# Kernel tuning notes

Measured on AMD Instinct MI355X. Metric: run time of the kernel, lower is better.

The kernel has to match this reference:

```python
import jax, jax.numpy as jnp
import numpy as np

N = 50000
E = 800000
NFEAT = 128
NHID = 64
NCLASS = 40


def setup_inputs() -> dict:
    key = jax.random.key(0)
    ks = jax.random.split(key, 12)
    return {
        "x": jax.random.normal(ks[0], (N, NFEAT), dtype=jnp.float32),
        "M": jax.random.uniform(ks[1], (N, 1), dtype=jnp.float32),
        "AM": jax.random.uniform(ks[2], (N, 1), dtype=jnp.float32),
        "adj_vals": jax.random.uniform(ks[3], (E,), dtype=jnp.float32),
        "adjZ_vals": jax.random.uniform(ks[4], (E,), dtype=jnp.float32),
        "W0": jax.random.normal(ks[5], (NFEAT, NFEAT), dtype=jnp.float32) * (1.414 / np.sqrt(NFEAT)),
        "b0": jnp.zeros((NFEAT,), dtype=jnp.float32),
        "W1": jax.random.normal(ks[6], (NFEAT, NHID), dtype=jnp.float32) * (1.414 / np.sqrt(NFEAT)),
        "b1": jnp.zeros((NHID,), dtype=jnp.float32),
        "W2": jax.random.normal(ks[7], (NHID, NCLASS), dtype=jnp.float32) * (1.0 / np.sqrt(NHID)),
        "b2": jnp.zeros((NCLASS,), dtype=jnp.float32),
        "row": jax.random.randint(ks[8], (E,), 0, N, dtype=jnp.int32),
        "col": jax.random.randint(ks[9], (E,), 0, N, dtype=jnp.int32),
    }


def _spmm(vals, row, col, X, n):
    # sparse (COO) @ dense: out[r] = sum_e vals[e] * X[col[e]] for row[e]==r
    return jax.ops.segment_sum(vals[:, None] * X[col], row, num_segments=n)


def reference(x, M, AM, adj_vals, adjZ_vals, W0, b0, W1, b1, W2, b2, row, col):
    n = x.shape[0]
    # gc0: PaGConv(nfeat->nfeat) on adjZ, then ReLU (dropout is identity in eval)
    h = _spmm(adjZ_vals, row, col, M * x, n) * AM
    h = jax.nn.relu(h @ W0 + b0)
    # gc1: PaGConv(nfeat->nhid) on adjZ, then ReLU
    h = _spmm(adjZ_vals, row, col, M * h, n) * AM
    h = jax.nn.relu(h @ W1 + b1)
    # gc2: plain GConv(nhid->nclass) on adj
    h = _spmm(adj_vals, row, col, h, n)
    h = h @ W2 + b2
    return jax.nn.log_softmax(h, axis=1)
```

## Files before the change

kernel.cpp:

```cpp
#include <hip/hip_runtime.h>
#include <hip/hip_bf16.h>
#include <math.h>


typedef __attribute__((ext_vector_type(8))) short bf16x8;
typedef __attribute__((ext_vector_type(4))) float f32x4;

#define HIST_EPB_LOG 15
#define HIST_EPB 32768
#define NBINS 50176
#define NBMAX 26
#define SCAN_BLOCKS 196

__device__ __forceinline__ float rl_f(float v, int j) {
    return __builtin_bit_cast(float,
        __builtin_amdgcn_readlane(__builtin_bit_cast(int, v), j));
}
__device__ __forceinline__ int rl_i(int v, int j) {
    return __builtin_amdgcn_readlane(v, j);
}
__device__ __forceinline__ unsigned short f2bf(float f) {
    unsigned u = __builtin_bit_cast(unsigned, f);
    u += 0x7fffu + ((u >> 16) & 1u);
    return (unsigned short)(u >> 16);
}
__device__ __forceinline__ unsigned pack2bf(float lo, float hi) {
    return (unsigned)f2bf(lo) | ((unsigned)f2bf(hi) << 16);
}
__device__ __forceinline__ float bf_lo(unsigned u) {
    return __builtin_bit_cast(float, u << 16);
}
__device__ __forceinline__ float bf_hi(unsigned u) {
    return __builtin_bit_cast(float, u & 0xffff0000u);
}
__device__ __forceinline__ float clampf(float v) {
    return fminf(fmaxf(v, -1e30f), 1e30f);
}


__global__ void prep_wt(const float* __restrict__ W0, const float* __restrict__ W1,
                        const float* __restrict__ W2,
                        unsigned short* __restrict__ wt0, unsigned short* __restrict__ wt1,
                        unsigned short* __restrict__ wt2) {
    int idx = blockIdx.x * 256 + threadIdx.x;
    if (idx < 128 * 128) {
        int nn = idx >> 7, k = idx & 127;
        wt0[idx] = f2bf(W0[k * 128 + nn]);
    }
    idx -= 128 * 128;
    if (idx >= 0 && idx < 64 * 128) {
        int nn = idx >> 7, k = idx & 127;
        wt1[idx] = f2bf(W1[k * 64 + nn]);
    }
    idx -= 64 * 128;
    if (idx >= 0 && idx < 48 * 64) {
        int nn = idx >> 6, k = idx & 63;
        wt2[idx] = (nn < 40) ? f2bf(W2[k * 40 + nn]) : (unsigned short)0;
    }
}


template <int K, int COLS, int NTPAD, bool ABF16, bool MSCALE>
__device__ __forceinline__ void gemm_mfma_body(const void* __restrict__ Asrc,
                                               const float* __restrict__ Mv,
                                               const unsigned short* __restrict__ Wt,
                                               unsigned short* __restrict__ outp,
                                               int n, int bid, int tid) {
    constexpr int KS = K / 32;
    const int lane = tid & 63;
    const int wid = tid >> 6;
    const int m15 = lane & 15;
    const int q = lane >> 4;
    const int rA = bid * 64 + wid * 16 + m15;

    bf16x8 a[KS];
    if constexpr (ABF16) {
        const unsigned short* A = (const unsigned short*)Asrc;
#pragma unroll
        for (int ks = 0; ks < KS; ++ks) {
            uint4 z = make_uint4(0u, 0u, 0u, 0u);
            if (rA < n) z = *(const uint4*)(A + (size_t)rA * K + ks * 32 + q * 8);
            a[ks] = __builtin_bit_cast(bf16x8, z);
        }
    } else {
        const float* A = (const float*)Asrc;
        float m = 1.0f;
        if constexpr (MSCALE) { if (rA < n) m = Mv[rA]; }
#pragma unroll
        for (int ks = 0; ks < KS; ++ks) {
            float4 lo = make_float4(0.f, 0.f, 0.f, 0.f);
            float4 hi = make_float4(0.f, 0.f, 0.f, 0.f);
            if (rA < n) {
                lo = *(const float4*)(A + (size_t)rA * K + ks * 32 + q * 8);
                hi = *(const float4*)(A + (size_t)rA * K + ks * 32 + q * 8 + 4);
            }
            union { bf16x8 v; unsigned short u[8]; } pk;
            pk.u[0] = f2bf(lo.x * m); pk.u[1] = f2bf(lo.y * m);
            pk.u[2] = f2bf(lo.z * m); pk.u[3] = f2bf(lo.w * m);
            pk.u[4] = f2bf(hi.x * m); pk.u[5] = f2bf(hi.y * m);
            pk.u[6] = f2bf(hi.z * m); pk.u[7] = f2bf(hi.w * m);
            a[ks] = pk.v;
        }
    }

#pragma unroll
    for (int nt = 0; nt < NTPAD / 16; ++nt) {
        f32x4 acc = {0.f, 0.f, 0.f, 0.f};
        const int bn = nt * 16 + m15;
#pragma unroll
        for (int ks = 0; ks < KS; ++ks) {
            const uint4 z = *(const uint4*)(Wt + (size_t)bn * K + ks * 32 + q * 8);
            const bf16x8 b = __builtin_bit_cast(bf16x8, z);
            acc = __builtin_amdgcn_mfma_f32_16x16x32_bf16(a[ks], b, acc, 0, 0, 0);
        }
        const int gc = nt * 16 + m15;
#pragma unroll
        for (int rr = 0; rr < 4; ++rr) {
            const int gr = bid * 64 + wid * 16 + q * 4 + rr;
            bool ok = gr < n;
            if constexpr (NTPAD != COLS) ok = ok && (gc < COLS);
            if (ok) outp[(size_t)gr * COLS + gc] = f2bf(clampf(acc[rr]));
        }
    }
}

template <int K, int COLS, int NTPAD, bool ABF16, bool MSCALE>
__launch_bounds__(256)
__global__ void gemm_mfma(const void* __restrict__ A, const float* __restrict__ Mv,
                          const unsigned short* __restrict__ Wt,
                          unsigned short* __restrict__ out, int n) {
    gemm_mfma_body<K, COLS, NTPAD, ABF16, MSCALE>(A, Mv, Wt, out, n, blockIdx.x,
                                                  threadIdx.x);
}


__launch_bounds__(1024)
__global__ void hist_gemm0(const int* __restrict__ row,
                           unsigned short* __restrict__ cntmat,
                           unsigned short* __restrict__ lrank, int E, int NB,
                           const float* __restrict__ x, const float* __restrict__ Mv,
                           const unsigned short* __restrict__ Wt0,
                           unsigned short* __restrict__ t_buf, int n) {
    __shared__ __align__(16) unsigned hcnt[NBINS / 2];
    const int blk = blockIdx.x;
    const int t = threadIdx.x;
    if (blk < NB) {
        uint4* h4 = (uint4*)hcnt;
        const uint4 z4 = make_uint4(0u, 0u, 0u, 0u);
        for (int i = t; i < NBINS / 8; i += 1024) h4[i] = z4;
        __syncthreads();
        const int s = blk << HIST_EPB_LOG;
        const int e = min(E, s + HIST_EPB);
        for (int i = s + t; i < e; i += 1024) {
            const int r = row[i];
            const unsigned sh = (unsigned)(r & 1) << 4;
            const unsigned old = atomicAdd(&hcnt[r >> 1], 1u << sh);
            lrank[i] = (unsigned short)((old >> sh) & 0xffffu);
        }
        __syncthreads();
        uint4* dst = (uint4*)(cntmat + (size_t)blk * NBINS);
        for (int i = t; i < NBINS / 8; i += 1024) dst[i] = h4[i];
    } else {
        const int sub = t >> 8;
        gemm_mfma_body<128, 128, 128, false, true>(x, Mv, Wt0, t_buf, n,
                                                   (blk - NB) * 4 + sub, t & 255);
    }
}


__launch_bounds__(256)
__global__ void scan_one(const unsigned short* __restrict__ cm,
                         unsigned* __restrict__ cmabs, int* __restrict__ rp,
                         unsigned long long* __restrict__ gpub,
                         int n, int NB, int E) {
    __shared__ int sd[256];
    const int g = blockIdx.x;
    const int t = threadIdx.x;
    const int bin = g * 256 + t;

    unsigned tot = 0;
    for (int b = 0; b < NB; ++b) tot += cm[(size_t)b * NBINS + bin];

    sd[t] = (int)tot;
    __syncthreads();
    for (int off = 1; off < 256; off <<= 1) {
        int xv = (t >= off) ? sd[t - off] : 0;
        __syncthreads();
        sd[t] += xv;
        __syncthreads();
    }
    const int excl = sd[t] - (int)tot;
    const int gtot = sd[255];
    __syncthreads();

    if (t == 0)
        atomicExch(&gpub[g], (1ULL << 32) | (unsigned long long)(unsigned)gtot);

    int my = 0;
    for (int p = t; p < g; p += 256) {
        unsigned long long v;
        do { v = atomicAdd(&gpub[p], 0ULL); } while ((v >> 32) == 0ULL);
        my += (int)(unsigned)v;
    }
    sd[t] = my;
    __syncthreads();
    for (int off = 128; off > 0; off >>= 1) {
        if (t < off) sd[t] += sd[t + off];
        __syncthreads();
    }
    const int base = sd[0];

    const int rpf = base + excl;
    if (bin < n) rp[bin] = rpf;
    if (g == SCAN_BLOCKS - 1 && t == 255) rp[n] = E;

    int run = rpf;
    for (int b = 0; b < NB; ++b) {
        cmabs[(size_t)b * NBINS + bin] = (unsigned)run;
        run += (int)cm[(size_t)b * NBINS + bin];
    }
}


__global__ void scatter_kernel(const int* __restrict__ row, const int* __restrict__ col,
                               const float* __restrict__ vA, const float* __restrict__ vZ,
                               const unsigned* __restrict__ cmabs,
                               const unsigned short* __restrict__ lrank,
                               uint4* __restrict__ packed16, int E) {
    int e = blockIdx.x * blockDim.x + threadIdx.x;
    if (e >= E) return;
    const int r = row[e];
    const int pos = (int)(cmabs[(size_t)(e >> HIST_EPB_LOG) * NBINS + r]
                          + (unsigned)lrank[e]);
    uint4 pk;
    pk.x = (unsigned)col[e];
    pk.y = __builtin_bit_cast(unsigned, vZ[e]);
    pk.z = __builtin_bit_cast(unsigned, vA[e]);
    pk.w = 0u;
    packed16[pos] = pk;
}


__launch_bounds__(256)
__global__ void spmm128_kernel(const uint4* __restrict__ packed16,
                               const int* __restrict__ rp, const unsigned short* __restrict__ X,
                               const float* __restrict__ AM, const float* __restrict__ Mv,
                               const float* __restrict__ bias,
                               unsigned short* __restrict__ out, int n) {
    const int lane = threadIdx.x & 63;
    const int r = (int)((blockIdx.x * (unsigned)blockDim.x + threadIdx.x) >> 6);
    if (r >= n) return;
    const int s = __builtin_amdgcn_readfirstlane(rp[r]);
    const int e = __builtin_amdgcn_readfirstlane(rp[r + 1]);

    float acc0 = 0.0f, acc1 = 0.0f;
    for (int base = s; base < e; base += 64) {
        const int nn = min(64, e - base);
        int ci = 0; float vf = 0.0f;
        if (lane < nn) {
            const uint4 pk = packed16[base + lane];
            ci = (int)pk.x;
            vf = __builtin_bit_cast(float, pk.y);
        }
        int j = 0;
        for (; j + 16 <= nn; j += 16) {
            unsigned u[16];
#pragma unroll
            for (int q = 0; q < 16; ++q) {
                const int cq = rl_i(ci, j + q);
                u[q] = *(const unsigned*)(X + (size_t)cq * 128 + lane * 2);
            }
#pragma unroll
            for (int q = 0; q < 16; ++q) {
                const float vq = rl_f(vf, j + q);
                acc0 += vq * bf_lo(u[q]);
                acc1 += vq * bf_hi(u[q]);
            }
        }
        for (; j + 8 <= nn; j += 8) {
            unsigned u[8];
#pragma unroll
            for (int q = 0; q < 8; ++q) {
                const int cq = rl_i(ci, j + q);
                u[q] = *(const unsigned*)(X + (size_t)cq * 128 + lane * 2);
            }
#pragma unroll
            for (int q = 0; q < 8; ++q) {
                const float vq = rl_f(vf, j + q);
                acc0 += vq * bf_lo(u[q]);
                acc1 += vq * bf_hi(u[q]);
            }
        }
        for (; j < nn; ++j) {
            const int cq = rl_i(ci, j);
            const float vq = rl_f(vf, j);
            const unsigned u = *(const unsigned*)(X + (size_t)cq * 128 + lane * 2);
            acc0 += vq * bf_lo(u);
            acc1 += vq * bf_hi(u);
        }
    }

    const float am = AM[r];
    const float mr = Mv[r];
    const float o0 = fminf(fmaxf((acc0 * am + bias[2 * lane]) * mr, 0.0f), 1e30f);
    const float o1 = fminf(fmaxf((acc1 * am + bias[2 * lane + 1]) * mr, 0.0f), 1e30f);
    ((unsigned*)out)[(size_t)r * 64 + lane] = pack2bf(o0, o1);
}


__launch_bounds__(256)
__global__ void spmm64_kernel(const uint4* __restrict__ packed16,
                              const int* __restrict__ rp, const unsigned short* __restrict__ X,
                              const float* __restrict__ AM, const float* __restrict__ bias,
                              unsigned short* __restrict__ out, int n) {
    const int lane = threadIdx.x & 63;
    const int g = lane >> 4;
    const int ls = lane & 15;
    const int r = (int)((blockIdx.x * (unsigned)blockDim.x + threadIdx.x) >> 6);
    if (r >= n) return;
    const int s = __builtin_amdgcn_readfirstlane(rp[r]);
    const int e = __builtin_amdgcn_readfirstlane(rp[r + 1]);

    float a0 = 0.0f, a1 = 0.0f, a2 = 0.0f, a3 = 0.0f;
    for (int base = s; base < e; base += 64) {
        const int nn = min(64, e - base);
        int ci = 0; float vf = 0.0f;
        if (lane < nn) {
            const uint4 pk = packed16[base + lane];
            ci = (int)pk.x;
            vf = __builtin_bit_cast(float, pk.y);
        }
        for (int j = 0; j < nn; j += 16) {
#pragma unroll
            for (int q = 0; q < 4; ++q) {
                const int jj = j + 4 * q + g;
                const bool ok = jj < nn;
                const int idx = jj & 63;
                const int c = __shfl(ci, idx);
                const float v = __shfl(vf, idx);
                if (ok) {
                    const uint2 u = *(const uint2*)(X + (size_t)c * 64 + ls * 4);
                    a0 += v * bf_lo(u.x);
                    a1 += v * bf_hi(u.x);
                    a2 += v * bf_lo(u.y);
                    a3 += v * bf_hi(u.y);
                }
            }
        }
    }
    a0 += __shfl_xor(a0, 16); a0 += __shfl_xor(a0, 32);
    a1 += __shfl_xor(a1, 16); a1 += __shfl_xor(a1, 32);
    a2 += __shfl_xor(a2, 16); a2 += __shfl_xor(a2, 32);
    a3 += __shfl_xor(a3, 16); a3 += __shfl_xor(a3, 32);

    if (lane < 16) {
        const float am = AM[r];
        const float o0 = fminf(fmaxf(a0 * am + bias[4 * ls + 0], 0.0f), 1e30f);
        const float o1 = fminf(fmaxf(a1 * am + bias[4 * ls + 1], 0.0f), 1e30f);
        const float o2 = fminf(fmaxf(a2 * am + bias[4 * ls + 2], 0.0f), 1e30f);
        const float o3 = fminf(fmaxf(a3 * am + bias[4 * ls + 3], 0.0f), 1e30f);
        uint2 w;
        w.x = pack2bf(o0, o1);
        w.y = pack2bf(o2, o3);
        *(uint2*)((unsigned*)out + (size_t)r * 32 + ls * 2) = w;
    }
}


__launch_bounds__(256)
__global__ void spmm40_kernel(const uint4* __restrict__ packed16,
                              const int* __restrict__ rp, const unsigned short* __restrict__ X,
                              const float* __restrict__ bias,
                              float* __restrict__ out, int n) {
    const int lane = threadIdx.x & 63;
    const int g = lane / 20;
    const int ls = lane - 20 * g;
    const bool active = g < 3;
    const int r = (int)((blockIdx.x * (unsigned)blockDim.x + threadIdx.x) >> 6);
    if (r >= n) return;
    const int s = __builtin_amdgcn_readfirstlane(rp[r]);
    const int e = __builtin_amdgcn_readfirstlane(rp[r + 1]);

    float acc0 = 0.0f, acc1 = 0.0f;
    for (int base = s; base < e; base += 64) {
        const int nn = min(64, e - base);
        int ci = 0; float vf = 0.0f;
        if (lane < nn) {
            const uint4 pk = packed16[base + lane];
            ci = (int)pk.x;
            vf = __builtin_bit_cast(float, pk.z);
        }
        for (int j = 0; j < nn; j += 24) {
#pragma unroll
            for (int q = 0; q < 8; ++q) {
                const int jj = j + 3 * q + g;
                const bool ok = active && jj < nn;
                const int idx = jj & 63;
                const int c = __shfl(ci, idx);
                const float v = __shfl(vf, idx);
                if (ok) {
                    const unsigned u = *(const unsigned*)(X + (size_t)c * 40 + ls * 2);
                    acc0 += v * bf_lo(u);
                    acc1 += v * bf_hi(u);
                }
            }
        }
    }
    {
        const float a1 = __shfl(acc0, (lane + 20) & 63);
        const float a2 = __shfl(acc0, (lane + 40) & 63);
        const float b1 = __shfl(acc1, (lane + 20) & 63);
        const float b2 = __shfl(acc1, (lane + 40) & 63);
        acc0 += a1 + a2;
        acc1 += b1 + b2;
    }

    const bool own = lane < 20;
    const float vv0 = own ? fminf(fmaxf(acc0 + bias[2 * ls], -1e30f), 1e30f) : -INFINITY;
    const float vv1 = own ? fminf(fmaxf(acc1 + bias[2 * ls + 1], -1e30f), 1e30f) : -INFINITY;
    float mx = fmaxf(vv0, vv1);
#pragma unroll
    for (int off = 32; off > 0; off >>= 1) mx = fmaxf(mx, __shfl_xor(mx, off));
    float sum = own ? (expf(vv0 - mx) + expf(vv1 - mx)) : 0.0f;
#pragma unroll
    for (int off = 32; off > 0; off >>= 1) sum += __shfl_xor(sum, off);
    if (own) {
        const float lse = mx + logf(sum);
        *(float2*)(out + (size_t)r * 40 + ls * 2) = make_float2(vv0 - lse, vv1 - lse);
    }
}


extern "C" void kernel_launch(void* const* d_in, const int* in_sizes, int n_in,
                              void* d_out, int out_size, void* d_ws, size_t ws_size,
                              hipStream_t stream) {
    const float* x    = (const float*)d_in[0];
    const float* M    = (const float*)d_in[1];
    const float* AM   = (const float*)d_in[2];
    const float* adjv = (const float*)d_in[3];
    const float* adjZ = (const float*)d_in[4];
    const float* W0   = (const float*)d_in[5];
    const float* b0   = (const float*)d_in[6];
    const float* W1   = (const float*)d_in[7];
    const float* b1   = (const float*)d_in[8];
    const float* W2   = (const float*)d_in[9];
    const float* b2   = (const float*)d_in[10];
    const int* row    = (const int*)d_in[11];
    const int* col    = (const int*)d_in[12];
    float* out = (float*)d_out;

    const int n = in_sizes[1];
    const int E = in_sizes[3];

    unsigned short* t_buf = (unsigned short*)d_ws;
    unsigned short* wt0 = t_buf + (size_t)n * 128;
    unsigned short* wt1 = wt0 + 128 * 128;
    unsigned short* wt2 = wt1 + 64 * 128;
    unsigned short* h_buf = wt2 + 48 * 64;
    unsigned short* lrank  = h_buf;
    unsigned short* cntmat = lrank + (size_t)E;
    unsigned* cmabs = (unsigned*)(cntmat + (size_t)NBMAX * NBINS);
    int* rp = (int*)(h_buf + (size_t)n * 128);
    unsigned long long* gpub = (unsigned long long*)
        (((uintptr_t)(rp + n + 2) + 7) & ~(uintptr_t)7);
    uint4* packed16 = (uint4*)
        (((uintptr_t)(gpub + 256) + 15) & ~(uintptr_t)15);

    const int NB = (E + HIST_EPB - 1) >> HIST_EPB_LOG;
    const int gemmBlocks = (n + 63) / 64;
    const int gemmB4 = (gemmBlocks + 3) / 4;

    hipMemsetAsync(gpub, 0, 256 * sizeof(unsigned long long), stream);
    prep_wt<<<(128 * 128 + 64 * 128 + 48 * 64 + 255) / 256, 256, 0, stream>>>(
        W0, W1, W2, wt0, wt1, wt2);

    hist_gemm0<<<NB + gemmB4, 1024, 0, stream>>>(row, cntmat, lrank, E, NB,
                                                 x, M, wt0, t_buf, n);

    scan_one<<<SCAN_BLOCKS, 256, 0, stream>>>(cntmat, cmabs, rp, gpub, n, NB, E);

    scatter_kernel<<<(E + 255) / 256, 256, 0, stream>>>(row, col, adjv, adjZ,
                                                        cmabs, lrank, packed16, E);

    const int spmmBlocks = (n + 3) / 4;

    spmm128_kernel<<<spmmBlocks, 256, 0, stream>>>(packed16, rp, t_buf, AM, M, b0, h_buf, n);
    gemm_mfma<128, 64, 64, true, false><<<gemmBlocks, 256, 0, stream>>>(h_buf, nullptr, wt1,
                                                                        t_buf, n);
    spmm64_kernel<<<spmmBlocks, 256, 0, stream>>>(packed16, rp, t_buf, AM, b1, h_buf, n);
    gemm_mfma<64, 40, 48, true, false><<<gemmBlocks, 256, 0, stream>>>(h_buf, nullptr, wt2,
                                                                       t_buf, n);
    spmm40_kernel<<<spmmBlocks, 256, 0, stream>>>(packed16, rp, t_buf, b2, out, n);
}
```

Baseline: 271.7 us.

## Fuse weight prep, scan+scatter, and spmm64 with gemm2 to cut launches

Folds the bf16 weight-transpose into block 0 of the histogram/gemm0 kernel, with the gemm0 blocks spin-waiting on a flag before reading the weights. Merges the prefix scan and the edge scatter into one persistent-style kernel that waits on a global counter. Fuses the final 64->40 projection into the spmm64 kernel using readlane broadcasts, so one gemm launch and one intermediate round-trip are dropped. Cross-block spin-waits rely on all blocks being co-resident or scheduled in order, which adds deadlock risk and some idle spinning.

```diff
diff --git a/kernel.cpp b/kernel.cpp
--- a/kernel.cpp
+++ b/kernel.cpp
@@ -11,6 +11,7 @@
 #define NBINS 50176
 #define NBMAX 26
 #define SCAN_BLOCKS 196
+#define SS_GRID 1568
 
 __device__ __forceinline__ float rl_f(float v, int j) {
     return __builtin_bit_cast(float,
@@ -38,34 +39,11 @@
 }
 
 
-__global__ void prep_wt(const float* __restrict__ W0, const float* __restrict__ W1,
-                        const float* __restrict__ W2,
-                        unsigned short* __restrict__ wt0, unsigned short* __restrict__ wt1,
-                        unsigned short* __restrict__ wt2) {
-    int idx = blockIdx.x * 256 + threadIdx.x;
-    if (idx < 128 * 128) {
-        int nn = idx >> 7, k = idx & 127;
-        wt0[idx] = f2bf(W0[k * 128 + nn]);
-    }
-    idx -= 128 * 128;
-    if (idx >= 0 && idx < 64 * 128) {
-        int nn = idx >> 7, k = idx & 127;
-        wt1[idx] = f2bf(W1[k * 64 + nn]);
-    }
-    idx -= 64 * 128;
-    if (idx >= 0 && idx < 48 * 64) {
-        int nn = idx >> 6, k = idx & 63;
-        wt2[idx] = (nn < 40) ? f2bf(W2[k * 40 + nn]) : (unsigned short)0;
-    }
-}
-
-
-template <int K, int COLS, int NTPAD, bool ABF16, bool MSCALE>
-__device__ __forceinline__ void gemm_mfma_body(const void* __restrict__ Asrc,
-                                               const float* __restrict__ Mv,
-                                               const unsigned short* __restrict__ Wt,
-                                               unsigned short* __restrict__ outp,
-                                               int n, int bid, int tid) {
+template <int K, int COLS, int NTPAD>
+__device__ __forceinline__ void gemm_mfma_body_bf16(const unsigned short* __restrict__ A,
+                                                    const unsigned short* __restrict__ Wt,
+                                                    unsigned short* __restrict__ outp,
+                                                    int n, int bid, int tid) {
     constexpr int KS = K / 32;
     const int lane = tid & 63;
     const int wid = tid >> 6;
@@ -74,33 +52,11 @@
     const int rA = bid * 64 + wid * 16 + m15;
 
     bf16x8 a[KS];
-    if constexpr (ABF16) {
-        const unsigned short* A = (const unsigned short*)Asrc;
-#pragma unroll
-        for (int ks = 0; ks < KS; ++ks) {
-            uint4 z = make_uint4(0u, 0u, 0u, 0u);
-            if (rA < n) z = *(const uint4*)(A + (size_t)rA * K + ks * 32 + q * 8);
-            a[ks] = __builtin_bit_cast(bf16x8, z);
-        }
-    } else {
-        const float* A = (const float*)Asrc;
-        float m = 1.0f;
-        if constexpr (MSCALE) { if (rA < n) m = Mv[rA]; }
-#pragma unroll
-        for (int ks = 0; ks < KS; ++ks) {
-            float4 lo = make_float4(0.f, 0.f, 0.f, 0.f);
-            float4 hi = make_float4(0.f, 0.f, 0.f, 0.f);
-            if (rA < n) {
-                lo = *(const float4*)(A + (size_t)rA * K + ks * 32 + q * 8);
-                hi = *(const float4*)(A + (size_t)rA * K + ks * 32 + q * 8 + 4);
-            }
-            union { bf16x8 v; unsigned short u[8]; } pk;
-            pk.u[0] = f2bf(lo.x * m); pk.u[1] = f2bf(lo.y * m);
-            pk.u[2] = f2bf(lo.z * m); pk.u[3] = f2bf(lo.w * m);
-            pk.u[4] = f2bf(hi.x * m); pk.u[5] = f2bf(hi.y * m);
-            pk.u[6] = f2bf(hi.z * m); pk.u[7] = f2bf(hi.w * m);
-            a[ks] = pk.v;
-        }
+#pragma unroll
+    for (int ks = 0; ks < KS; ++ks) {
+        uint4 z = make_uint4(0u, 0u, 0u, 0u);
+        if (rA < n) z = *(const uint4*)(A + (size_t)rA * K + ks * 32 + q * 8);
+        a[ks] = __builtin_bit_cast(bf16x8, z);
     }
 
 #pragma unroll
@@ -110,8 +66,8 @@
 #pragma unroll
         for (int ks = 0; ks < KS; ++ks) {
             const uint4 z = *(const uint4*)(Wt + (size_t)bn * K + ks * 32 + q * 8);
-            const bf16x8 b = __builtin_bit_cast(bf16x8, z);
-            acc = __builtin_amdgcn_mfma_f32_16x16x32_bf16(a[ks], b, acc, 0, 0, 0);
+            acc = __builtin_amdgcn_mfma_f32_16x16x32_bf16(
+                a[ks], __builtin_bit_cast(bf16x8, z), acc, 0, 0, 0);
         }
         const int gc = nt * 16 + m15;
 #pragma unroll
@@ -124,13 +80,12 @@
     }
 }
 
-template <int K, int COLS, int NTPAD, bool ABF16, bool MSCALE>
+template <int K, int COLS, int NTPAD>
 __launch_bounds__(256)
-__global__ void gemm_mfma(const void* __restrict__ A, const float* __restrict__ Mv,
+__global__ void gemm_mfma(const unsigned short* __restrict__ A,
                           const unsigned short* __restrict__ Wt,
                           unsigned short* __restrict__ out, int n) {
-    gemm_mfma_body<K, COLS, NTPAD, ABF16, MSCALE>(A, Mv, Wt, out, n, blockIdx.x,
-                                                  threadIdx.x);
+    gemm_mfma_body_bf16<K, COLS, NTPAD>(A, Wt, out, n, blockIdx.x, threadIdx.x);
 }
 
 
@@ -139,17 +94,38 @@
                            unsigned short* __restrict__ cntmat,
                            unsigned short* __restrict__ lrank, int E, int NB,
                            const float* __restrict__ x, const float* __restrict__ Mv,
-                           const unsigned short* __restrict__ Wt0,
-                           unsigned short* __restrict__ t_buf, int n) {
+                           const float* __restrict__ W0, const float* __restrict__ W1,
+                           const float* __restrict__ W2,
+                           unsigned short* __restrict__ wt0,
+                           unsigned short* __restrict__ wt1,
+                           unsigned short* __restrict__ wt2,
+                           unsigned short* __restrict__ t_buf,
+                           unsigned long long* __restrict__ gpub, int n) {
     __shared__ __align__(16) unsigned hcnt[NBINS / 2];
     const int blk = blockIdx.x;
     const int t = threadIdx.x;
-    if (blk < NB) {
+    if (blk == 0) {
+        for (int idx = t; idx < 128 * 128; idx += 1024) {
+            int nn = idx >> 7, k = idx & 127;
+            wt0[idx] = f2bf(W0[k * 128 + nn]);
+        }
+        for (int idx = t; idx < 64 * 128; idx += 1024) {
+            int nn = idx >> 7, k = idx & 127;
+            wt1[idx] = f2bf(W1[k * 64 + nn]);
+        }
+        for (int idx = t; idx < 48 * 64; idx += 1024) {
+            int nn = idx >> 6, k = idx & 63;
+            wt2[idx] = (nn < 40) ? f2bf(W2[k * 40 + nn]) : (unsigned short)0;
+        }
+        __threadfence();
+        __syncthreads();
+        if (t == 0) atomicExch(&gpub[255], 1ULL);
+    } else if (blk <= NB) {
         uint4* h4 = (uint4*)hcnt;
         const uint4 z4 = make_uint4(0u, 0u, 0u, 0u);
         for (int i = t; i < NBINS / 8; i += 1024) h4[i] = z4;
         __syncthreads();
-        const int s = blk << HIST_EPB_LOG;
+        const int s = (blk - 1) << HIST_EPB_LOG;
         const int e = min(E, s + HIST_EPB);
         for (int i = s + t; i < e; i += 1024) {
             const int r = row[i];
@@ -158,86 +134,145 @@
             lrank[i] = (unsigned short)((old >> sh) & 0xffffu);
         }
         __syncthreads();
-        uint4* dst = (uint4*)(cntmat + (size_t)blk * NBINS);
+        uint4* dst = (uint4*)(cntmat + (size_t)(blk - 1) * NBINS);
         for (int i = t; i < NBINS / 8; i += 1024) dst[i] = h4[i];
     } else {
-        const int sub = t >> 8;
-        gemm_mfma_body<128, 128, 128, false, true>(x, Mv, Wt0, t_buf, n,
-                                                   (blk - NB) * 4 + sub, t & 255);
-    }
-}
-
-
-__launch_bounds__(256)
-__global__ void scan_one(const unsigned short* __restrict__ cm,
-                         unsigned* __restrict__ cmabs, int* __restrict__ rp,
-                         unsigned long long* __restrict__ gpub,
-                         int n, int NB, int E) {
+        const int tid = t & 255;
+        const int bid = (blk - 1 - NB) * 4 + (t >> 8);
+        const int lane = tid & 63;
+        const int wid = tid >> 6;
+        const int m15 = lane & 15;
+        const int q = lane >> 4;
+        const int rA = bid * 64 + wid * 16 + m15;
+
+        bf16x8 a[4];
+        {
+            float m = 1.0f;
+            if (rA < n) m = Mv[rA];
+#pragma unroll
+            for (int ks = 0; ks < 4; ++ks) {
+                float4 lo = make_float4(0.f, 0.f, 0.f, 0.f);
+                float4 hi = make_float4(0.f, 0.f, 0.f, 0.f);
+                if (rA < n) {
+                    lo = *(const float4*)(x + (size_t)rA * 128 + ks * 32 + q * 8);
+                    hi = *(const float4*)(x + (size_t)rA * 128 + ks * 32 + q * 8 + 4);
+                }
+                union { bf16x8 v; unsigned short u[8]; } pk;
+                pk.u[0] = f2bf(lo.x * m); pk.u[1] = f2bf(lo.y * m);
+                pk.u[2] = f2bf(lo.z * m); pk.u[3] = f2bf(lo.w * m);
+                pk.u[4] = f2bf(hi.x * m); pk.u[5] = f2bf(hi.y * m);
+                pk.u[6] = f2bf(hi.z * m); pk.u[7] = f2bf(hi.w * m);
+                a[ks] = pk.v;
+            }
+        }
+        if (t == 0) {
+            while (atomicAdd(&gpub[255], 0ULL) == 0ULL) __builtin_amdgcn_s_sleep(2);
+        }
+        __syncthreads();
+        __threadfence();
+#pragma unroll
+        for (int nt = 0; nt < 8; ++nt) {
+            f32x4 acc = {0.f, 0.f, 0.f, 0.f};
+            const int bn = nt * 16 + m15;
+#pragma unroll
+            for (int ks = 0; ks < 4; ++ks) {
+                const uint4 z = *(const uint4*)(wt0 + (size_t)bn * 128 + ks * 32 + q * 8);
+                acc = __builtin_amdgcn_mfma_f32_16x16x32_bf16(
+                    a[ks], __builtin_bit_cast(bf16x8, z), acc, 0, 0, 0);
+            }
+            const int gc = nt * 16 + m15;
+#pragma unroll
+            for (int rr = 0; rr < 4; ++rr) {
+                const int gr = bid * 64 + wid * 16 + q * 4 + rr;
+                if (gr < n) t_buf[(size_t)gr * 128 + gc] = f2bf(clampf(acc[rr]));
+            }
+        }
+    }
+}
+
+
+__launch_bounds__(256, 8)
+__global__ void scan_scatter(const unsigned short* __restrict__ cm,
+                             unsigned* __restrict__ cmabs, int* __restrict__ rp,
+                             unsigned long long* __restrict__ gpub,
+                             const int* __restrict__ row, const int* __restrict__ col,
+                             const float* __restrict__ vA, const float* __restrict__ vZ,
+                             const unsigned short* __restrict__ lrank,
+                             uint4* __restrict__ packed16,
+                             int n, int NB, int E) {
     __shared__ int sd[256];
     const int g = blockIdx.x;
     const int t = threadIdx.x;
-    const int bin = g * 256 + t;
-
-    unsigned tot = 0;
-    for (int b = 0; b < NB; ++b) tot += cm[(size_t)b * NBINS + bin];
-
-    sd[t] = (int)tot;
+
+    if (g < SCAN_BLOCKS) {
+        const int bin = g * 256 + t;
+        unsigned tot = 0;
+        for (int b = 0; b < NB; ++b) tot += cm[(size_t)b * NBINS + bin];
+
+        sd[t] = (int)tot;
+        __syncthreads();
+        for (int off = 1; off < 256; off <<= 1) {
+            int xv = (t >= off) ? sd[t - off] : 0;
+            __syncthreads();
+            sd[t] += xv;
+            __syncthreads();
+        }
+        const int excl = sd[t] - (int)tot;
+        const int gtot = sd[255];
+        __syncthreads();
+
+        if (t == 0)
+            atomicExch(&gpub[g], (1ULL << 32) | (unsigned long long)(unsigned)gtot);
+
+        int my = 0;
+        for (int p = t; p < g; p += 256) {
+            unsigned long long v;
+            do { v = atomicAdd(&gpub[p], 0ULL); } while ((v >> 32) == 0ULL);
+            my += (int)(unsigned)v;
+        }
+        sd[t] = my;
+        __syncthreads();
+        for (int off = 128; off > 0; off >>= 1) {
+            if (t < off) sd[t] += sd[t + off];
+            __syncthreads();
+        }
+        const int base = sd[0];
+
+        const int rpf = base + excl;
+        if (bin < n) rp[bin] = rpf;
+        if (g == 0 && t == 0) rp[n] = E;
+
+        int run = rpf;
+        for (int b = 0; b < NB; ++b) {
+            cmabs[(size_t)b * NBINS + bin] = (unsigned)run;
+            run += (int)cm[(size_t)b * NBINS + bin];
+        }
+        __threadfence();
+        __syncthreads();
+        if (t == 0) atomicAdd(&gpub[254], 1ULL);
+    }
+
+    if (t == 0) {
+        while (atomicAdd(&gpub[254], 0ULL) < (unsigned long long)SCAN_BLOCKS)
+            __builtin_amdgcn_s_sleep(2);
+    }
     __syncthreads();
-    for (int off = 1; off < 256; off <<= 1) {
-        int xv = (t >= off) ? sd[t - off] : 0;
-        __syncthreads();
-        sd[t] += xv;
-        __syncthreads();
-    }
-    const int excl = sd[t] - (int)tot;
-    const int gtot = sd[255];
-    __syncthreads();
-
-    if (t == 0)
-        atomicExch(&gpub[g], (1ULL << 32) | (unsigned long long)(unsigned)gtot);
-
-    int my = 0;
-    for (int p = t; p < g; p += 256) {
-        unsigned long long v;
-        do { v = atomicAdd(&gpub[p], 0ULL); } while ((v >> 32) == 0ULL);
-        my += (int)(unsigned)v;
-    }
-    sd[t] = my;
-    __syncthreads();
-    for (int off = 128; off > 0; off >>= 1) {
-        if (t < off) sd[t] += sd[t + off];
-        __syncthreads();
-    }
-    const int base = sd[0];
-
-    const int rpf = base + excl;
-    if (bin < n) rp[bin] = rpf;
-    if (g == SCAN_BLOCKS - 1 && t == 255) rp[n] = E;
-
-    int run = rpf;
-    for (int b = 0; b < NB; ++b) {
-        cmabs[(size_t)b * NBINS + bin] = (unsigned)run;
-        run += (int)cm[(size_t)b * NBINS + bin];
-    }
-}
-
-
-__global__ void scatter_kernel(const int* __restrict__ row, const int* __restrict__ col,
-                               const float* __restrict__ vA, const float* __restrict__ vZ,
-                               const unsigned* __restrict__ cmabs,
-                               const unsigned short* __restrict__ lrank,
-                               uint4* __restrict__ packed16, int E) {
-    int e = blockIdx.x * blockDim.x + threadIdx.x;
-    if (e >= E) return;
-    const int r = row[e];
-    const int pos = (int)(cmabs[(size_t)(e >> HIST_EPB_LOG) * NBINS + r]
-                          + (unsigned)lrank[e]);
-    uint4 pk;
-    pk.x = (unsigned)col[e];
-    pk.y = __builtin_bit_cast(unsigned, vZ[e]);
-    pk.z = __builtin_bit_cast(unsigned, vA[e]);
-    pk.w = 0u;
-    packed16[pos] = pk;
+    __threadfence();
+
+    const int ce = (E + SS_GRID - 1) / SS_GRID;
+    const int s0 = g * ce;
+    const int s1 = min(E, s0 + ce);
+    for (int i = s0 + t; i < s1; i += 256) {
+        const int r = row[i];
+        const int pos = (int)(cmabs[(size_t)(i >> HIST_EPB_LOG) * NBINS + r]
+                              + (unsigned)lrank[i]);
+        uint4 pk;
+        pk.x = (unsigned)col[i];
+        pk.y = __builtin_bit_cast(unsigned, vZ[i]);
+        pk.z = __builtin_bit_cast(unsigned, vA[i]);
+        pk.w = 0u;
+        packed16[pos] = pk;
+    }
 }
 
 
@@ -309,10 +344,11 @@
 
 
 __launch_bounds__(256)
-__global__ void spmm64_kernel(const uint4* __restrict__ packed16,
-                              const int* __restrict__ rp, const unsigned short* __restrict__ X,
-                              const float* __restrict__ AM, const float* __restrict__ bias,
-                              unsigned short* __restrict__ out, int n) {
+__global__ void spmm64_gemm2(const uint4* __restrict__ packed16,
+                             const int* __restrict__ rp, const unsigned short* __restrict__ X,
+                             const float* __restrict__ AM, const float* __restrict__ bias1,
+                             const unsigned short* __restrict__ wt2,
+                             unsigned short* __restrict__ out40, int n) {
     const int lane = threadIdx.x & 63;
     const int g = lane >> 4;
     const int ls = lane & 15;
@@ -353,17 +389,26 @@
     a2 += __shfl_xor(a2, 16); a2 += __shfl_xor(a2, 32);
     a3 += __shfl_xor(a3, 16); a3 += __shfl_xor(a3, 32);
 
-    if (lane < 16) {
-        const float am = AM[r];
-        const float o0 = fminf(fmaxf(a0 * am + bias[4 * ls + 0], 0.0f), 1e30f);
-        const float o1 = fminf(fmaxf(a1 * am + bias[4 * ls + 1], 0.0f), 1e30f);
-        const float o2 = fminf(fmaxf(a2 * am + bias[4 * ls + 2], 0.0f), 1e30f);
-        const float o3 = fminf(fmaxf(a3 * am + bias[4 * ls + 3], 0.0f), 1e30f);
-        uint2 w;
-        w.x = pack2bf(o0, o1);
-        w.y = pack2bf(o2, o3);
-        *(uint2*)((unsigned*)out + (size_t)r * 32 + ls * 2) = w;
-    }
+    const float am = AM[r];
+    const float o0 = fminf(fmaxf(a0 * am + bias1[4 * ls + 0], 0.0f), 1e30f);
+    const float o1 = fminf(fmaxf(a1 * am + bias1[4 * ls + 1], 0.0f), 1e30f);
+    const float o2 = fminf(fmaxf(a2 * am + bias1[4 * ls + 2], 0.0f), 1e30f);
+    const float o3 = fminf(fmaxf(a3 * am + bias1[4 * ls + 3], 0.0f), 1e30f);
+
+    const int wrow = (lane < 48) ? lane : 0;
+    const unsigned short* wp = wt2 + wrow * 64;
+    float y = 0.0f;
+#pragma unroll
+    for (int qq = 0; qq < 16; ++qq) {
+        const uint2 w = *(const uint2*)(wp + 4 * qq);
+        const float h0v = rl_f(o0, qq);
+        const float h1v = rl_f(o1, qq);
+        const float h2v = rl_f(o2, qq);
+        const float h3v = rl_f(o3, qq);
+        y += h0v * bf_lo(w.x) + h1v * bf_hi(w.x)
+           + h2v * bf_lo(w.y) + h3v * bf_hi(w.y);
+    }
+    if (lane < 40) out40[(size_t)r * 40 + lane] = f2bf(clampf(y));
 }
 
 
@@ -471,24 +516,19 @@
     const int gemmB4 = (gemmBlocks + 3) / 4;
 
     hipMemsetAsync(gpub, 0, 256 * sizeof(unsigned long long), stream);
-    prep_wt<<<(128 * 128 + 64 * 128 + 48 * 64 + 255) / 256, 256, 0, stream>>>(
-        W0, W1, W2, wt0, wt1, wt2);
-
-    hist_gemm0<<<NB + gemmB4, 1024, 0, stream>>>(row, cntmat, lrank, E, NB,
-                                                 x, M, wt0, t_buf, n);
-
-    scan_one<<<SCAN_BLOCKS, 256, 0, stream>>>(cntmat, cmabs, rp, gpub, n, NB, E);
-
-    scatter_kernel<<<(E + 255) / 256, 256, 0, stream>>>(row, col, adjv, adjZ,
-                                                        cmabs, lrank, packed16, E);
+
+    hist_gemm0<<<1 + NB + gemmB4, 1024, 0, stream>>>(row, cntmat, lrank, E, NB,
+                                                     x, M, W0, W1, W2,
+                                                     wt0, wt1, wt2, t_buf, gpub, n);
+
+    scan_scatter<<<SS_GRID, 256, 0, stream>>>(cntmat, cmabs, rp, gpub,
+                                              row, col, adjv, adjZ, lrank,
+                                              packed16, n, NB, E);
 
     const int spmmBlocks = (n + 3) / 4;
 
     spmm128_kernel<<<spmmBlocks, 256, 0, stream>>>(packed16, rp, t_buf, AM, M, b0, h_buf, n);
-    gemm_mfma<128, 64, 64, true, false><<<gemmBlocks, 256, 0, stream>>>(h_buf, nullptr, wt1,
-                                                                        t_buf, n);
-    spmm64_kernel<<<spmmBlocks, 256, 0, stream>>>(packed16, rp, t_buf, AM, b1, h_buf, n);
-    gemm_mfma<64, 40, 48, true, false><<<gemmBlocks, 256, 0, stream>>>(h_buf, nullptr, wt2,
-                                                                       t_buf, n);
-    spmm40_kernel<<<spmmBlocks, 256, 0, stream>>>(packed16, rp, t_buf, b2, out, n);
-}
+    gemm_mfma<128, 64, 64><<<gemmBlocks, 256, 0, stream>>>(h_buf, wt1, t_buf, n);
+    spmm64_gemm2<<<spmmBlocks, 256, 0, stream>>>(packed16, rp, t_buf, AM, b1, wt2, h_buf, n);
+    spmm40_kernel<<<spmmBlocks, 256, 0, stream>>>(packed16, rp, h_buf, b2, out, n);
+}
```

After: 465.3 us. 71.3% more time.
